# Performance work log

Measured on AMD Instinct MI355X. Metric: run time of the kernel, lower is better.

## Reference

```python
import jax, jax.numpy as jnp
import numpy as np

# hparams (match init_kwargs)
EXP_LOW_BOUND = -8.0          # clip scores-max to [low_bound, 0]
EXP_CLIP_AND_SUBTRACT = True  # subtract exp(low_bound) from clipped tensor before exp
EXP_LINEAR_GRADIENT = 0.0     # 0 -> use true exp on the clipped/shifted tensor
EXP_SUM_HIGH_BOUND = 1024.0   # clamp the softmax denominator
RECIP_LINEAR_GRADIENT = 0.0   # 0 -> exact reciprocal
RECIP_LOW_BOUND = 0.0

B, S, H, D = 4, 1024, 16, 64


def _approx_exp(x):
    # exponential() from the source
    if EXP_LOW_BOUND != 0:
        x = jnp.clip(x, EXP_LOW_BOUND, 0.0)
    if EXP_CLIP_AND_SUBTRACT:
        x = x - np.float32(np.exp(EXP_LOW_BOUND))
    if EXP_LINEAR_GRADIENT:
        return jnp.clip(x * np.float32(EXP_LINEAR_GRADIENT) + 1.0, 0.0, 1.0)
    return jnp.exp(x)


def _approx_recip(x):
    # reciprocal() from the source
    if RECIP_LINEAR_GRADIENT != 0:
        g = np.float32(RECIP_LINEAR_GRADIENT)
        return jnp.clip((1.0 + g) - g * x, RECIP_LOW_BOUND, 1.0)
    return 1.0 / x


def _custom_softmax(a):
    # softmax() with exp_hparams / reciprocal_hparams path, norm over last axis
    amax = jnp.max(a, axis=-1, keepdims=True)
    amax = jnp.where(jnp.isfinite(amax), amax, 0.0)
    asubmax = a - amax
    approx_exp = _approx_exp(asubmax)                       # [B,H,Sq,Sk]
    asumexp = jnp.sum(approx_exp, axis=-1, keepdims=True)   # [B,H,Sq,1]
    if EXP_SUM_HIGH_BOUND:
        sum_low_bound = 1.0
        if EXP_LOW_BOUND != 0 and EXP_CLIP_AND_SUBTRACT:
            sum_low_bound = 1.0 - float(np.exp(EXP_LOW_BOUND))
        asumexp = jnp.clip(asumexp, sum_low_bound, EXP_SUM_HIGH_BOUND)
    return approx_exp * _approx_recip(asumexp)


def setup_inputs() -> dict:
    key = jax.random.key(0)
    kq, kk, kv = jax.random.split(key, 3)
    return {
        "query": jax.random.normal(kq, (B, S, H, D), dtype=jnp.float32),
        "key": jax.random.normal(kk, (B, S, H, D), dtype=jnp.float32),
        "value": jax.random.normal(kv, (B, S, H, D), dtype=jnp.float32),
    }


def reference(query, key, value):
    depth = query.shape[-1]
    q = query * (1.0 / np.sqrt(depth)).astype(np.float32)
    # scores: [B, H, Sq, Sk]
    scores = jnp.einsum("bqhd,bkhd->bhqk", q, key)
    weights = _custom_softmax(scores).astype(query.dtype)
    # output: [B, Sq, H, D]
    return jnp.einsum("bhqk,bkhd->bqhd", weights, value)
```

## Files before the change

kernel.cpp:

```cpp
#include <hip/hip_runtime.h>

#define BB 4
#define SS 1024
#define HH 16
#define DD 64

typedef short bf16x8 __attribute__((ext_vector_type(8)));
typedef float f32x4 __attribute__((ext_vector_type(4)));

__device__ __forceinline__ unsigned pk2(float a, float b) {
    unsigned ua = __float_as_uint(a) + 0x8000u;
    unsigned ub = __float_as_uint(b) + 0x8000u;
    return (ub & 0xffff0000u) | (ua >> 16);
}
__device__ __forceinline__ unsigned short f2bf(float a) {
    return (unsigned short)((__float_as_uint(a) + 0x8000u) >> 16);
}
__device__ __forceinline__ f32x4 mfma16(bf16x8 a, bf16x8 b, f32x4 c) {
    return __builtin_amdgcn_mfma_f32_16x16x32_bf16(a, b, c, 0, 0, 0);
}
__device__ __forceinline__ int sig5(int x) {
    int a = (x >> 4) & 1, qs = (x >> 2) & 3, b2 = x & 3;
    return ((qs ^ (b2 >> 1)) << 3) | (a << 2) | b2;
}

__global__ __launch_bounds__(256)
void prep_kernel(const float* __restrict__ k, const float* __restrict__ v,
                 unsigned short* __restrict__ kws, unsigned short* __restrict__ vws) {
    const int t = threadIdx.x;
    const int bx = blockIdx.x;
    if (bx < 512) {
        const int bh = bx & 63, st = bx >> 6;
        const int h = bh & 15, b = bh >> 4;
        const int row = t >> 1, half = t & 1;
        const int p = st * 128 + row;
        const int key = (p & ~31) | sig5(p & 31);
        const float4* src = (const float4*)k + (((size_t)(b * SS + key) * HH + h) * 16) + half * 8;
        float4 r[8];
        #pragma unroll
        for (int i = 0; i < 8; ++i) r[i] = src[i];
        const int c32 = st * 4 + (row >> 5);
        const int f   = ((row >> 4) & 1) * 2 + half;
        const int n16k = row & 15;
        uint4* dst = (uint4*)(kws + (size_t)bh * 65536 + (size_t)((c32 * 4 + f) * 512 + n16k * 32));
        #pragma unroll
        for (int u = 0; u < 4; ++u) {
            uint4 val;
            val.x = pk2(r[2*u].x, r[2*u].y);
            val.y = pk2(r[2*u].z, r[2*u].w);
            val.z = pk2(r[2*u+1].x, r[2*u+1].y);
            val.w = pk2(r[2*u+1].z, r[2*u+1].w);
            dst[u] = val;
        }
    } else {
        const int bx2 = bx - 512;
        const int bh = bx2 & 63, st = bx2 >> 6;
        const int h = bh & 15, b = bh >> 4;
        const int o = t >> 4, vc = t & 15;
        const float4* src = (const float4*)v + (((size_t)(b * SS + st * 128 + o * 8) * HH + h) * 16) + vc;
        float4 r[8];
        #pragma unroll
        for (int i = 0; i < 8; ++i) r[i] = src[(size_t)i * HH * 16];
        const float* fr = (const float*)r;
        const int c32 = st * 4 + (o >> 2);
        const int quad = o & 3;
        #pragma unroll
        for (int c = 0; c < 4; ++c) {
            const int d = 4 * vc + c;
            const int dt = d >> 4, n16v = d & 15;
            uint4 val;
            val.x = pk2(fr[0*4+c], fr[1*4+c]);
            val.y = pk2(fr[2*4+c], fr[3*4+c]);
            val.z = pk2(fr[4*4+c], fr[5*4+c]);
            val.w = pk2(fr[6*4+c], fr[7*4+c]);
            *(uint4*)(vws + (size_t)bh * 65536 +
                      (size_t)((c32 * 4 + dt) * 512 + quad * 128 + n16v * 8)) = val;
        }
    }
}

#define ISSUE_KV(K0,K1,K2,K3,V0,V1,V2,V3, vk, vv)                                            \
  asm volatile("global_load_dwordx4 %0, %1, %2 offset:0"    : "=v"(K0) : "v"(vk), "s"(kb));  \
  asm volatile("global_load_dwordx4 %0, %1, %2 offset:1024" : "=v"(K1) : "v"(vk), "s"(kb));  \
  asm volatile("global_load_dwordx4 %0, %1, %2 offset:2048" : "=v"(K2) : "v"(vk), "s"(kb));  \
  asm volatile("global_load_dwordx4 %0, %1, %2 offset:3072" : "=v"(K3) : "v"(vk), "s"(kb));  \
  asm volatile("global_load_dwordx4 %0, %1, %2 offset:0"    : "=v"(V0) : "v"(vv), "s"(vbb)); \
  asm volatile("global_load_dwordx4 %0, %1, %2 offset:1024" : "=v"(V1) : "v"(vv), "s"(vbb)); \
  asm volatile("global_load_dwordx4 %0, %1, %2 offset:2048" : "=v"(V2) : "v"(vv), "s"(vbb)); \
  asm volatile("global_load_dwordx4 %0, %1, %2 offset:3072" : "=v"(V3) : "v"(vv), "s"(vbb));

#define WAIT_KV(K0,K1,K2,K3,V0,V1,V2,V3)                                  \
  asm volatile("s_waitcnt vmcnt(0)"                                       \
    : "+v"(K0),"+v"(K1),"+v"(K2),"+v"(K3),                                \
      "+v"(V0),"+v"(V1),"+v"(V2),"+v"(V3));

__device__ __forceinline__ void step32v(bf16x8 K0, bf16x8 K1, bf16x8 K2, bf16x8 K3,
                                        bf16x8 V0, bf16x8 V1, bf16x8 V2, bf16x8 V3,
                                        const bf16x8 qf[2][2],
                                        f32x4 oacc[2][4], float su[2]) {
    const f32x4 zero = {0.f, 0.f, 0.f, 0.f};
    const float LOG2E = 1.44269504f;
    f32x4 S[2][2];
    S[0][0] = mfma16(K1, qf[0][1], mfma16(K0, qf[0][0], zero));
    S[1][0] = mfma16(K1, qf[1][1], mfma16(K0, qf[1][0], zero));
    S[0][1] = mfma16(K3, qf[0][1], mfma16(K2, qf[0][0], zero));
    S[1][1] = mfma16(K3, qf[1][1], mfma16(K2, qf[1][0], zero));
    #pragma unroll
    for (int s = 0; s < 2; ++s) {
        unsigned P0[2], P1[2];
        #pragma unroll
        for (int ct = 0; ct < 2; ++ct) {
            float e0 = __builtin_amdgcn_exp2f(S[s][ct][0] * LOG2E);
            float e1 = __builtin_amdgcn_exp2f(S[s][ct][1] * LOG2E);
            float e2 = __builtin_amdgcn_exp2f(S[s][ct][2] * LOG2E);
            float e3 = __builtin_amdgcn_exp2f(S[s][ct][3] * LOG2E);
            su[s] += (e0 + e1) + (e2 + e3);
            P0[ct] = pk2(e0, e1);
            P1[ct] = pk2(e2, e3);
        }
        union { uint4 u; bf16x8 f; } pf;
        pf.u.x = P0[0];
        pf.u.y = (unsigned)__shfl_xor((int)P1[0], 16);
        pf.u.z = P0[1];
        pf.u.w = (unsigned)__shfl_xor((int)P1[1], 16);
        #pragma unroll
        for (int dt = 0; dt < 4; ++dt) {
            bf16x8 vv = dt == 0 ? V0 : dt == 1 ? V1 : dt == 2 ? V2 : V3;
            oacc[s][dt] = mfma16(vv, pf.f, oacc[s][dt]);
        }
    }
}

__global__ __launch_bounds__(256, 2)
void attn_stream(const float* __restrict__ q, const unsigned short* __restrict__ kws,
                 const unsigned short* __restrict__ vws, float* __restrict__ out) {
    const int t = threadIdx.x, lane = t & 63, w = t >> 6;
    const int n16 = lane & 15, quad = lane >> 4;
    const int bx = blockIdx.x;
    const int bh = bx & 63, qt = bx >> 6;
    const int h = bh & 15, b = bh >> 4;
    const int qbase = qt * 128 + w * 32;

    bf16x8 qf[2][2];
    #pragma unroll
    for (int s = 0; s < 2; ++s)
      #pragma unroll
      for (int ks = 0; ks < 2; ++ks) {
        const float* p = q + (((size_t)(b * SS + qbase + s * 16 + n16) * HH + h) * DD)
                           + ks * 32 + quad * 8;
        float4 x = ((const float4*)p)[0];
        float4 y = ((const float4*)p)[1];
        bf16x8 f;
        f[0] = (short)f2bf(x.x * 0.125f); f[1] = (short)f2bf(x.y * 0.125f);
        f[2] = (short)f2bf(x.z * 0.125f); f[3] = (short)f2bf(x.w * 0.125f);
        f[4] = (short)f2bf(y.x * 0.125f); f[5] = (short)f2bf(y.y * 0.125f);
        f[6] = (short)f2bf(y.z * 0.125f); f[7] = (short)f2bf(y.w * 0.125f);
        qf[s][ks] = f;
      }

    const unsigned short* kb  = kws + (size_t)bh * 65536;
    const unsigned short* vbb = vws + (size_t)bh * 65536;

    f32x4 oacc[2][4];
    #pragma unroll
    for (int s = 0; s < 2; ++s)
      #pragma unroll
      for (int dt = 0; dt < 4; ++dt) oacc[s][dt] = f32x4{0.f, 0.f, 0.f, 0.f};
    float su[2] = {0.f, 0.f};

    const unsigned basek = ((unsigned)n16 << 6) | ((unsigned)quad << 4);
    const unsigned basev = ((unsigned)quad << 8) | ((unsigned)n16 << 4);

    bf16x8 Ka0, Ka1, Ka2, Ka3, Va0, Va1, Va2, Va3;
    bf16x8 Kb0, Kb1, Kb2, Kb3, Vb0, Vb1, Vb2, Vb3;

    ISSUE_KV(Ka0,Ka1,Ka2,Ka3,Va0,Va1,Va2,Va3, basek, basev)
    WAIT_KV(Ka0,Ka1,Ka2,Ka3,Va0,Va1,Va2,Va3)

    #pragma unroll 1
    for (int it = 0; it < 16; ++it) {
        const unsigned c1 = (unsigned)(it * 2 + 1) << 12;
        ISSUE_KV(Kb0,Kb1,Kb2,Kb3,Vb0,Vb1,Vb2,Vb3, basek + c1, basev + c1)
        step32v(Ka0,Ka1,Ka2,Ka3,Va0,Va1,Va2,Va3, qf, oacc, su);
        WAIT_KV(Kb0,Kb1,Kb2,Kb3,Vb0,Vb1,Vb2,Vb3)

        const unsigned c2 = (unsigned)((it * 2 + 2) & 31) << 12;
        ISSUE_KV(Ka0,Ka1,Ka2,Ka3,Va0,Va1,Va2,Va3, basek + c2, basev + c2)
        step32v(Kb0,Kb1,Kb2,Kb3,Vb0,Vb1,Vb2,Vb3, qf, oacc, su);
        WAIT_KV(Ka0,Ka1,Ka2,Ka3,Va0,Va1,Va2,Va3)
    }

    #pragma unroll
    for (int s = 0; s < 2; ++s) {
        su[s] += __shfl_xor(su[s], 16);
        su[s] += __shfl_xor(su[s], 32);
    }
    #pragma unroll
    for (int s = 0; s < 2; ++s) {
        float sc = 1.0f / su[s];
        #pragma unroll
        for (int dt = 0; dt < 4; ++dt) {
            float4 val;
            val.x = oacc[s][dt][0] * sc;
            val.y = oacc[s][dt][1] * sc;
            val.z = oacc[s][dt][2] * sc;
            val.w = oacc[s][dt][3] * sc;
            size_t off = ((size_t)(b * SS + qbase + s * 16 + n16) * HH + h) * DD
                       + dt * 16 + quad * 4;
            *(float4*)&out[off] = val;
        }
    }
}

extern "C" void kernel_launch(void* const* d_in, const int* in_sizes, int n_in,
                              void* d_out, int out_size, void* d_ws, size_t ws_size,
                              hipStream_t stream) {
    const float* q = (const float*)d_in[0];
    const float* k = (const float*)d_in[1];
    const float* v = (const float*)d_in[2];
    float* o = (float*)d_out;
    unsigned short* kws = (unsigned short*)d_ws;
    unsigned short* vws = kws + (size_t)64 * 65536;
    hipLaunchKernelGGL(prep_kernel, dim3(1024), dim3(256), 0, stream, k, v, kws, vws);
    hipLaunchKernelGGL(attn_stream, dim3(512), dim3(256), 0, stream, q, kws, vws, o);
}
```

Before: 123.3 us.

## Stage K/V chunks through LDS with async global_load_lds ring buffer

Replaces each wave's direct per-lane global loads of K/V fragments with a four-slot LDS ring filled by global_load_lds, three chunks ahead. The four waves of a block now share one copy of each K/V chunk instead of each fetching it redundantly, and the prep kernel writes an XOR-swizzled layout so the LDS fragment reads avoid bank conflicts. This cuts global/L2 traffic by about a factor of four and deepens the prefetch, but adds a block-wide barrier every iteration and uses 32 KB of LDS.

```diff
diff --git a/kernel.cpp b/kernel.cpp
--- a/kernel.cpp
+++ b/kernel.cpp
@@ -22,6 +22,9 @@
 __device__ __forceinline__ int sig5(int x) {
     int a = (x >> 4) & 1, qs = (x >> 2) & 3, b2 = x & 3;
     return ((qs ^ (b2 >> 1)) << 3) | (a << 2) | b2;
+}
+__device__ __forceinline__ unsigned swz1k(unsigned o) {
+    return o ^ (((o >> 7) & 7u) << 4);
 }
 
 __global__ __launch_bounds__(256)
@@ -42,7 +45,7 @@
         const int c32 = st * 4 + (row >> 5);
         const int f   = ((row >> 4) & 1) * 2 + half;
         const int n16k = row & 15;
-        uint4* dst = (uint4*)(kws + (size_t)bh * 65536 + (size_t)((c32 * 4 + f) * 512 + n16k * 32));
+        char* bp = (char*)(kws + (size_t)bh * 65536) + (size_t)((c32 * 4 + f) * 1024);
         #pragma unroll
         for (int u = 0; u < 4; ++u) {
             uint4 val;
@@ -50,7 +53,8 @@
             val.y = pk2(r[2*u].z, r[2*u].w);
             val.z = pk2(r[2*u+1].x, r[2*u+1].y);
             val.w = pk2(r[2*u+1].z, r[2*u+1].w);
-            dst[u] = val;
+            unsigned o = swz1k(((unsigned)n16k << 6) | ((unsigned)u << 4));
+            *(uint4*)(bp + o) = val;
         }
     } else {
         const int bx2 = bx - 512;
@@ -73,26 +77,12 @@
             val.y = pk2(fr[2*4+c], fr[3*4+c]);
             val.z = pk2(fr[4*4+c], fr[5*4+c]);
             val.w = pk2(fr[6*4+c], fr[7*4+c]);
-            *(uint4*)(vws + (size_t)bh * 65536 +
-                      (size_t)((c32 * 4 + dt) * 512 + quad * 128 + n16v * 8)) = val;
-        }
-    }
-}
-
-#define ISSUE_KV(K0,K1,K2,K3,V0,V1,V2,V3, vk, vv)                                            \
-  asm volatile("global_load_dwordx4 %0, %1, %2 offset:0"    : "=v"(K0) : "v"(vk), "s"(kb));  \
-  asm volatile("global_load_dwordx4 %0, %1, %2 offset:1024" : "=v"(K1) : "v"(vk), "s"(kb));  \
-  asm volatile("global_load_dwordx4 %0, %1, %2 offset:2048" : "=v"(K2) : "v"(vk), "s"(kb));  \
-  asm volatile("global_load_dwordx4 %0, %1, %2 offset:3072" : "=v"(K3) : "v"(vk), "s"(kb));  \
-  asm volatile("global_load_dwordx4 %0, %1, %2 offset:0"    : "=v"(V0) : "v"(vv), "s"(vbb)); \
-  asm volatile("global_load_dwordx4 %0, %1, %2 offset:1024" : "=v"(V1) : "v"(vv), "s"(vbb)); \
-  asm volatile("global_load_dwordx4 %0, %1, %2 offset:2048" : "=v"(V2) : "v"(vv), "s"(vbb)); \
-  asm volatile("global_load_dwordx4 %0, %1, %2 offset:3072" : "=v"(V3) : "v"(vv), "s"(vbb));
-
-#define WAIT_KV(K0,K1,K2,K3,V0,V1,V2,V3)                                  \
-  asm volatile("s_waitcnt vmcnt(0)"                                       \
-    : "+v"(K0),"+v"(K1),"+v"(K2),"+v"(K3),                                \
-      "+v"(V0),"+v"(V1),"+v"(V2),"+v"(V3));
+            char* bp = (char*)(vws + (size_t)bh * 65536) + (size_t)((c32 * 4 + dt) * 1024);
+            unsigned oo = swz1k(((unsigned)quad << 8) | ((unsigned)n16v << 4));
+            *(uint4*)(bp + oo) = val;
+        }
+    }
+}
 
 __device__ __forceinline__ void step32v(bf16x8 K0, bf16x8 K1, bf16x8 K2, bf16x8 K3,
                                         bf16x8 V0, bf16x8 V1, bf16x8 V2, bf16x8 V3,
@@ -134,6 +124,8 @@
 __global__ __launch_bounds__(256, 2)
 void attn_stream(const float* __restrict__ q, const unsigned short* __restrict__ kws,
                  const unsigned short* __restrict__ vws, float* __restrict__ out) {
+    __shared__ __align__(16) unsigned short ldsbuf[16384];
+
     const int t = threadIdx.x, lane = t & 63, w = t >> 6;
     const int n16 = lane & 15, quad = lane >> 4;
     const int bx = blockIdx.x;
@@ -170,25 +162,46 @@
 
     const unsigned basek = ((unsigned)n16 << 6) | ((unsigned)quad << 4);
     const unsigned basev = ((unsigned)quad << 8) | ((unsigned)n16 << 4);
-
-    bf16x8 Ka0, Ka1, Ka2, Ka3, Va0, Va1, Va2, Va3;
-    bf16x8 Kb0, Kb1, Kb2, Kb3, Vb0, Vb1, Vb2, Vb3;
-
-    ISSUE_KV(Ka0,Ka1,Ka2,Ka3,Va0,Va1,Va2,Va3, basek, basev)
-    WAIT_KV(Ka0,Ka1,Ka2,Ka3,Va0,Va1,Va2,Va3)
+    const unsigned okK = swz1k(basek);
+    const unsigned okV = swz1k(basev);
+
+    const unsigned gsl = (unsigned)(w * 512 + lane * 8);
+    const unsigned lslK = (unsigned)(w * 512);
+    const unsigned lslV = (unsigned)(2048 + w * 512);
+
+#define STAGE(slot, chunk) do {                                                      \
+    const unsigned short* gk_ = kb  + (unsigned)(chunk) * 2048u + gsl;               \
+    const unsigned short* gv_ = vbb + (unsigned)(chunk) * 2048u + gsl;               \
+    __builtin_amdgcn_global_load_lds(                                                \
+        (const __attribute__((address_space(1))) void*)gk_,                          \
+        (__attribute__((address_space(3))) void*)(ldsbuf + (slot) * 4096 + lslK),    \
+        16, 0, 0);                                                                   \
+    __builtin_amdgcn_global_load_lds(                                                \
+        (const __attribute__((address_space(1))) void*)gv_,                          \
+        (__attribute__((address_space(3))) void*)(ldsbuf + (slot) * 4096 + lslV),    \
+        16, 0, 0);                                                                   \
+} while (0)
+
+    STAGE(0, 0); STAGE(1, 1); STAGE(2, 2);
 
     #pragma unroll 1
-    for (int it = 0; it < 16; ++it) {
-        const unsigned c1 = (unsigned)(it * 2 + 1) << 12;
-        ISSUE_KV(Kb0,Kb1,Kb2,Kb3,Vb0,Vb1,Vb2,Vb3, basek + c1, basev + c1)
-        step32v(Ka0,Ka1,Ka2,Ka3,Va0,Va1,Va2,Va3, qf, oacc, su);
-        WAIT_KV(Kb0,Kb1,Kb2,Kb3,Vb0,Vb1,Vb2,Vb3)
-
-        const unsigned c2 = (unsigned)((it * 2 + 2) & 31) << 12;
-        ISSUE_KV(Ka0,Ka1,Ka2,Ka3,Va0,Va1,Va2,Va3, basek + c2, basev + c2)
-        step32v(Kb0,Kb1,Kb2,Kb3,Vb0,Vb1,Vb2,Vb3, qf, oacc, su);
-        WAIT_KV(Ka0,Ka1,Ka2,Ka3,Va0,Va1,Va2,Va3)
-    }
+    for (int it = 0; it < 32; ++it) {
+        asm volatile("s_waitcnt vmcnt(4)\n\ts_barrier" ::: "memory");
+        STAGE((it + 3) & 3, (it + 3) & 31);
+
+        const char* sb = (const char*)ldsbuf + (it & 3) * 8192;
+        bf16x8 K0 = *(const bf16x8*)(sb + okK);
+        bf16x8 K1 = *(const bf16x8*)(sb + okK + 1024);
+        bf16x8 K2 = *(const bf16x8*)(sb + okK + 2048);
+        bf16x8 K3 = *(const bf16x8*)(sb + okK + 3072);
+        bf16x8 V0 = *(const bf16x8*)(sb + okV + 4096);
+        bf16x8 V1 = *(const bf16x8*)(sb + okV + 5120);
+        bf16x8 V2 = *(const bf16x8*)(sb + okV + 6144);
+        bf16x8 V3 = *(const bf16x8*)(sb + okV + 7168);
+        step32v(K0, K1, K2, K3, V0, V1, V2, V3, qf, oacc, su);
+    }
+#undef STAGE
+    asm volatile("s_waitcnt vmcnt(0)" ::: "memory");
 
     #pragma unroll
     for (int s = 0; s < 2; ++s) {
```

After: 121.9 us. Within noise of the previous version (-1.1%).

## Fuse K/V bf16 conversion into attention kernel via swizzled LDS ring

Applied to the files above, without the earlier changes.

Removes the separate prep kernel that converted K and V to bf16 in a workspace layout. The attention kernel now loads fp32 K and V cooperatively per block, converts and packs them, and writes them into a 4-slot swizzled LDS ring buffer with barriers. Each wave then reads its MFMA fragments from LDS. This drops one launch and the workspace round trip through global memory. In exchange, every query-tile block redoes the K/V conversion, and the kernel adds LDS traffic and a barrier on every step, with only a quarter of threads loading V.

```diff
diff --git a/kernel.cpp b/kernel.cpp
--- a/kernel.cpp
+++ b/kernel.cpp
@@ -1,6 +1,5 @@
 #include <hip/hip_runtime.h>
 
-#define BB 4
 #define SS 1024
 #define HH 16
 #define DD 64
@@ -23,76 +22,9 @@
     int a = (x >> 4) & 1, qs = (x >> 2) & 3, b2 = x & 3;
     return ((qs ^ (b2 >> 1)) << 3) | (a << 2) | b2;
 }
-
-__global__ __launch_bounds__(256)
-void prep_kernel(const float* __restrict__ k, const float* __restrict__ v,
-                 unsigned short* __restrict__ kws, unsigned short* __restrict__ vws) {
-    const int t = threadIdx.x;
-    const int bx = blockIdx.x;
-    if (bx < 512) {
-        const int bh = bx & 63, st = bx >> 6;
-        const int h = bh & 15, b = bh >> 4;
-        const int row = t >> 1, half = t & 1;
-        const int p = st * 128 + row;
-        const int key = (p & ~31) | sig5(p & 31);
-        const float4* src = (const float4*)k + (((size_t)(b * SS + key) * HH + h) * 16) + half * 8;
-        float4 r[8];
-        #pragma unroll
-        for (int i = 0; i < 8; ++i) r[i] = src[i];
-        const int c32 = st * 4 + (row >> 5);
-        const int f   = ((row >> 4) & 1) * 2 + half;
-        const int n16k = row & 15;
-        uint4* dst = (uint4*)(kws + (size_t)bh * 65536 + (size_t)((c32 * 4 + f) * 512 + n16k * 32));
-        #pragma unroll
-        for (int u = 0; u < 4; ++u) {
-            uint4 val;
-            val.x = pk2(r[2*u].x, r[2*u].y);
-            val.y = pk2(r[2*u].z, r[2*u].w);
-            val.z = pk2(r[2*u+1].x, r[2*u+1].y);
-            val.w = pk2(r[2*u+1].z, r[2*u+1].w);
-            dst[u] = val;
-        }
-    } else {
-        const int bx2 = bx - 512;
-        const int bh = bx2 & 63, st = bx2 >> 6;
-        const int h = bh & 15, b = bh >> 4;
-        const int o = t >> 4, vc = t & 15;
-        const float4* src = (const float4*)v + (((size_t)(b * SS + st * 128 + o * 8) * HH + h) * 16) + vc;
-        float4 r[8];
-        #pragma unroll
-        for (int i = 0; i < 8; ++i) r[i] = src[(size_t)i * HH * 16];
-        const float* fr = (const float*)r;
-        const int c32 = st * 4 + (o >> 2);
-        const int quad = o & 3;
-        #pragma unroll
-        for (int c = 0; c < 4; ++c) {
-            const int d = 4 * vc + c;
-            const int dt = d >> 4, n16v = d & 15;
-            uint4 val;
-            val.x = pk2(fr[0*4+c], fr[1*4+c]);
-            val.y = pk2(fr[2*4+c], fr[3*4+c]);
-            val.z = pk2(fr[4*4+c], fr[5*4+c]);
-            val.w = pk2(fr[6*4+c], fr[7*4+c]);
-            *(uint4*)(vws + (size_t)bh * 65536 +
-                      (size_t)((c32 * 4 + dt) * 512 + quad * 128 + n16v * 8)) = val;
-        }
-    }
-}
-
-#define ISSUE_KV(K0,K1,K2,K3,V0,V1,V2,V3, vk, vv)                                            \
-  asm volatile("global_load_dwordx4 %0, %1, %2 offset:0"    : "=v"(K0) : "v"(vk), "s"(kb));  \
-  asm volatile("global_load_dwordx4 %0, %1, %2 offset:1024" : "=v"(K1) : "v"(vk), "s"(kb));  \
-  asm volatile("global_load_dwordx4 %0, %1, %2 offset:2048" : "=v"(K2) : "v"(vk), "s"(kb));  \
-  asm volatile("global_load_dwordx4 %0, %1, %2 offset:3072" : "=v"(K3) : "v"(vk), "s"(kb));  \
-  asm volatile("global_load_dwordx4 %0, %1, %2 offset:0"    : "=v"(V0) : "v"(vv), "s"(vbb)); \
-  asm volatile("global_load_dwordx4 %0, %1, %2 offset:1024" : "=v"(V1) : "v"(vv), "s"(vbb)); \
-  asm volatile("global_load_dwordx4 %0, %1, %2 offset:2048" : "=v"(V2) : "v"(vv), "s"(vbb)); \
-  asm volatile("global_load_dwordx4 %0, %1, %2 offset:3072" : "=v"(V3) : "v"(vv), "s"(vbb));
-
-#define WAIT_KV(K0,K1,K2,K3,V0,V1,V2,V3)                                  \
-  asm volatile("s_waitcnt vmcnt(0)"                                       \
-    : "+v"(K0),"+v"(K1),"+v"(K2),"+v"(K3),                                \
-      "+v"(V0),"+v"(V1),"+v"(V2),"+v"(V3));
+__device__ __forceinline__ unsigned swz1k(unsigned o) {
+    return o ^ (((o >> 7) & 7u) << 4);
+}
 
 __device__ __forceinline__ void step32v(bf16x8 K0, bf16x8 K1, bf16x8 K2, bf16x8 K3,
                                         bf16x8 V0, bf16x8 V1, bf16x8 V2, bf16x8 V3,
@@ -132,14 +64,29 @@
 }
 
 __global__ __launch_bounds__(256, 2)
-void attn_stream(const float* __restrict__ q, const unsigned short* __restrict__ kws,
-                 const unsigned short* __restrict__ vws, float* __restrict__ out) {
+void attn_fused(const float* __restrict__ q, const float* __restrict__ k,
+                const float* __restrict__ v, float* __restrict__ out) {
+    __shared__ __align__(16) unsigned short ldsbuf[16384];
+
     const int t = threadIdx.x, lane = t & 63, w = t >> 6;
     const int n16 = lane & 15, quad = lane >> 4;
     const int bx = blockIdx.x;
     const int bh = bx & 63, qt = bx >> 6;
     const int h = bh & 15, b = bh >> 4;
     const int qbase = qt * 128 + w * 32;
+
+    const int kx = t >> 3, khalf = (t >> 2) & 1, ku = t & 3;
+    const int kf = ((kx >> 4) & 1) * 2 + khalf;
+    const unsigned kwoff = (unsigned)(kf * 1024)
+                         + swz1k((unsigned)((kx & 15) * 64 + ku * 16));
+    const int ksig = sig5(kx);
+    const bool vact = (t & 3) == 0;
+    const int vtid = t >> 2, vo = vtid >> 4, vvc = vtid & 15;
+
+    const float4* kbase = (const float4*)k + ((size_t)(b * SS) * HH + h) * 16
+                        + khalf * 8 + 2 * ku;
+    const float4* vbase = (const float4*)v + ((size_t)(b * SS + vo * 8) * HH + h) * 16
+                        + vvc;
 
     bf16x8 qf[2][2];
     #pragma unroll
@@ -158,9 +105,6 @@
         qf[s][ks] = f;
       }
 
-    const unsigned short* kb  = kws + (size_t)bh * 65536;
-    const unsigned short* vbb = vws + (size_t)bh * 65536;
-
     f32x4 oacc[2][4];
     #pragma unroll
     for (int s = 0; s < 2; ++s)
@@ -168,27 +112,79 @@
       for (int dt = 0; dt < 4; ++dt) oacc[s][dt] = f32x4{0.f, 0.f, 0.f, 0.f};
     float su[2] = {0.f, 0.f};
 
-    const unsigned basek = ((unsigned)n16 << 6) | ((unsigned)quad << 4);
-    const unsigned basev = ((unsigned)quad << 8) | ((unsigned)n16 << 4);
-
-    bf16x8 Ka0, Ka1, Ka2, Ka3, Va0, Va1, Va2, Va3;
-    bf16x8 Kb0, Kb1, Kb2, Kb3, Vb0, Vb1, Vb2, Vb3;
-
-    ISSUE_KV(Ka0,Ka1,Ka2,Ka3,Va0,Va1,Va2,Va3, basek, basev)
-    WAIT_KV(Ka0,Ka1,Ka2,Ka3,Va0,Va1,Va2,Va3)
+    const unsigned okK = swz1k(((unsigned)n16 << 6) | ((unsigned)quad << 4));
+    const unsigned okV = swz1k(((unsigned)quad << 8) | ((unsigned)n16 << 4));
+
+#define ISSUE(c, kr, vr) do {                                                    \
+    const float4* ks_ = kbase + (size_t)((c) * 32 + ksig) * (HH * 16);           \
+    kr[0] = ks_[0]; kr[1] = ks_[1];                                              \
+    if (vact) {                                                                  \
+        const float4* vs_ = vbase + (size_t)(c) * 32 * (HH * 16);                \
+        _Pragma("unroll")                                                        \
+        for (int kk_ = 0; kk_ < 8; ++kk_) vr[kk_] = vs_[kk_ * (HH * 16)];        \
+    }                                                                            \
+} while (0)
+
+#define WRITE(slot, kr, vr) do {                                                 \
+    char* sb_ = (char*)ldsbuf + (slot) * 8192;                                   \
+    uint4 kv_;                                                                   \
+    kv_.x = pk2(kr[0].x, kr[0].y); kv_.y = pk2(kr[0].z, kr[0].w);                \
+    kv_.z = pk2(kr[1].x, kr[1].y); kv_.w = pk2(kr[1].z, kr[1].w);                \
+    *(uint4*)(sb_ + kwoff) = kv_;                                                \
+    if (vact) {                                                                  \
+        const float* fr_ = (const float*)vr;                                     \
+        _Pragma("unroll")                                                        \
+        for (int cc_ = 0; cc_ < 4; ++cc_) {                                      \
+            const int d_ = 4 * vvc + cc_;                                        \
+            uint4 q4_;                                                           \
+            q4_.x = pk2(fr_[0*4+cc_], fr_[1*4+cc_]);                             \
+            q4_.y = pk2(fr_[2*4+cc_], fr_[3*4+cc_]);                             \
+            q4_.z = pk2(fr_[4*4+cc_], fr_[5*4+cc_]);                             \
+            q4_.w = pk2(fr_[6*4+cc_], fr_[7*4+cc_]);                             \
+            *(uint4*)(sb_ + 4096 + (d_ >> 4) * 1024 +                            \
+                      swz1k((unsigned)(vo * 256 + (d_ & 15) * 16))) = q4_;       \
+        }                                                                        \
+    }                                                                            \
+} while (0)
+
+#define BAR asm volatile("s_waitcnt lgkmcnt(0)\n\ts_barrier" ::: "memory")
+
+#define COMPUTE(slot) do {                                                       \
+    const char* cb_ = (const char*)ldsbuf + (slot) * 8192;                       \
+    bf16x8 K0 = *(const bf16x8*)(cb_ + okK);                                     \
+    bf16x8 K1 = *(const bf16x8*)(cb_ + okK + 1024);                              \
+    bf16x8 K2 = *(const bf16x8*)(cb_ + okK + 2048);                              \
+    bf16x8 K3 = *(const bf16x8*)(cb_ + okK + 3072);                              \
+    bf16x8 V0 = *(const bf16x8*)(cb_ + okV + 4096);                              \
+    bf16x8 V1 = *(const bf16x8*)(cb_ + okV + 5120);                              \
+    bf16x8 V2 = *(const bf16x8*)(cb_ + okV + 6144);                              \
+    bf16x8 V3 = *(const bf16x8*)(cb_ + okV + 7168);                              \
+    step32v(K0, K1, K2, K3, V0, V1, V2, V3, qf, oacc, su);                       \
+} while (0)
+
+    float4 krA[2], vrA[8], krB[2], vrB[8];
+
+    ISSUE(0, krA, vrA);
+    WRITE(0, krA, vrA);
+    ISSUE(1, krB, vrB);
+    BAR;
 
     #pragma unroll 1
-    for (int it = 0; it < 16; ++it) {
-        const unsigned c1 = (unsigned)(it * 2 + 1) << 12;
-        ISSUE_KV(Kb0,Kb1,Kb2,Kb3,Vb0,Vb1,Vb2,Vb3, basek + c1, basev + c1)
-        step32v(Ka0,Ka1,Ka2,Ka3,Va0,Va1,Va2,Va3, qf, oacc, su);
-        WAIT_KV(Kb0,Kb1,Kb2,Kb3,Vb0,Vb1,Vb2,Vb3)
-
-        const unsigned c2 = (unsigned)((it * 2 + 2) & 31) << 12;
-        ISSUE_KV(Ka0,Ka1,Ka2,Ka3,Va0,Va1,Va2,Va3, basek + c2, basev + c2)
-        step32v(Kb0,Kb1,Kb2,Kb3,Vb0,Vb1,Vb2,Vb3, qf, oacc, su);
-        WAIT_KV(Ka0,Ka1,Ka2,Ka3,Va0,Va1,Va2,Va3)
-    }
+    for (int it2 = 0; it2 < 16; ++it2) {
+        const int it = it2 * 2;
+        WRITE((it + 1) & 3, krB, vrB);
+        { const int c_ = (it + 2 < 32) ? it + 2 : 31; ISSUE(c_, krA, vrA); }
+        BAR;
+        COMPUTE(it & 3);
+        WRITE((it + 2) & 3, krA, vrA);
+        { const int c_ = (it + 3 < 32) ? it + 3 : 31; ISSUE(c_, krB, vrB); }
+        BAR;
+        COMPUTE((it + 1) & 3);
+    }
+#undef ISSUE
+#undef WRITE
+#undef BAR
+#undef COMPUTE
 
     #pragma unroll
     for (int s = 0; s < 2; ++s) {
@@ -219,8 +215,6 @@
     const float* k = (const float*)d_in[1];
     const float* v = (const float*)d_in[2];
     float* o = (float*)d_out;
-    unsigned short* kws = (unsigned short*)d_ws;
-    unsigned short* vws = kws + (size_t)64 * 65536;
-    hipLaunchKernelGGL(prep_kernel, dim3(1024), dim3(256), 0, stream, k, v, kws, vws);
-    hipLaunchKernelGGL(attn_stream, dim3(512), dim3(256), 0, stream, q, kws, vws, o);
-}
+    (void)d_ws; (void)ws_size;
+    hipLaunchKernelGGL(attn_fused, dim3(512), dim3(256), 0, stream, q, k, v, o);
+}
```

Result: no change. 123.7 us (+0.4%).
